# Performance work log

Hardware: AMD Instinct MI355X
Metric: run time of the kernel (lower is better)

The kernel has to match this reference:

```python
import jax, jax.numpy as jnp
import numpy as np

N = 100000   # nodes
E = 1600000  # edges
D_IN = 128
D = 128
G = 64       # graphs in batch
C = 2        # out_channels
EPS = 1e-5   # BatchNorm eps


def setup_inputs() -> dict:
    key = jax.random.key(0)
    ks = jax.random.split(key, 24)
    s = 0.05
    inp = {
        "x": jax.random.normal(ks[0], (N, D_IN), dtype=jnp.float32),
        "edge_index": jax.random.randint(ks[1], (2, E), 0, N, dtype=jnp.int32),
        "edge_attr": jax.random.uniform(ks[2], (E, 2), dtype=jnp.float32),
        "batch": jnp.sort(jax.random.randint(ks[3], (N,), 0, G, dtype=jnp.int32)),
        # GCN layer 0
        "Wg0": jax.random.normal(ks[4], (D_IN, D), dtype=jnp.float32) * s,
        "bg0": jnp.zeros((D,), jnp.float32),
        "gamma0": jnp.ones((D,), jnp.float32),
        "beta0": jnp.zeros((D,), jnp.float32),
        # GCN layer 1
        "Wg1": jax.random.normal(ks[5], (D, D), dtype=jnp.float32) * s,
        "bg1": jnp.zeros((D,), jnp.float32),
        "gamma1": jnp.ones((D,), jnp.float32),
        "beta1": jnp.zeros((D,), jnp.float32),
        # dense head
        "Wl1": jax.random.normal(ks[6], (D, D), dtype=jnp.float32) * s,
        "bl1": jnp.zeros((D,), jnp.float32),
        "Wl2": jax.random.normal(ks[7], (D, D), dtype=jnp.float32) * s,
        "bl2": jnp.zeros((D,), jnp.float32),
        "Wc1": jax.random.normal(ks[8], (D, D), dtype=jnp.float32) * s,
        "bc1": jnp.zeros((D,), jnp.float32),
        "Wc2": jax.random.normal(ks[9], (D, C), dtype=jnp.float32) * s,
        "bc2": jnp.zeros((C,), jnp.float32),
    }
    return inp


def _gcn_conv(x, src, dst, w, W, b):
    # PyG GCNConv: h = x @ W ; add self-loops (weight 1) ; symmetric norm ; agg at dst ; + bias
    h = x @ W                                                   # [N, D]
    deg = jax.ops.segment_sum(w, dst, num_segments=N) + 1.0     # self-loop weight 1
    dinv = jnp.where(deg > 0, jax.lax.rsqrt(deg), 0.0)          # deg^{-1/2}
    norm = dinv[src] * w * dinv[dst]                            # [E]
    agg = jax.ops.segment_sum(norm[:, None] * h[src], dst, num_segments=N)
    agg = agg + (dinv * dinv)[:, None] * h                      # self-loop contribution
    return agg + b


def _bn(x, gamma, beta):
    # training-mode batch statistics over the node dimension
    m = x.mean(axis=0)
    v = x.var(axis=0)
    return (x - m) * jax.lax.rsqrt(v + EPS) * gamma + beta


def reference(x, edge_index, edge_attr, batch,
              Wg0, bg0, gamma0, beta0,
              Wg1, bg1, gamma1, beta1,
              Wl1, bl1, Wl2, bl2, Wc1, bc1, Wc2, bc2):
    src, dst = edge_index[0], edge_index[1]
    w = edge_attr[:, 1]  # which_edge_weight is None -> column 1

    h = jax.nn.relu(_gcn_conv(x, src, dst, w, Wg0, bg0))
    h = _bn(h, gamma0, beta0)                 # dropout: identity (eval)
    h = jax.nn.relu(_gcn_conv(h, src, dst, w, Wg1, bg1))
    h = _bn(h, gamma1, beta1)

    h = jax.nn.relu(h @ Wl1 + bl1)
    h = h @ Wl2 + bl2                          # node embeddings [N, D]

    counts = jax.ops.segment_sum(jnp.ones((N,), h.dtype), batch, num_segments=G)
    graph_reps = jax.ops.segment_sum(h, batch, num_segments=G) / jnp.maximum(counts, 1.0)[:, None]

    logits = jax.nn.relu(graph_reps @ Wc1 + bc1) @ Wc2 + bc2   # [G, C]
    return (h, graph_reps, logits)
```

## Files before the change

### kernel.cpp

```cpp
#include <hip/hip_runtime.h>

#define N_NODES 100000
#define N_EDGES 1600000
#define DFEAT   128
#define NGRAPH  64
#define EPSV    1e-5f
#define SCAN_BLOCKS ((N_NODES + 255) / 256)
#define DEG_SCALE 268435456.0f
#define DEG_MASK  ((1ULL << 42) - 1)

typedef float v4f  __attribute__((ext_vector_type(4)));
typedef short v8s  __attribute__((ext_vector_type(8)));
typedef unsigned short us4 __attribute__((ext_vector_type(4)));
typedef unsigned short us8 __attribute__((ext_vector_type(8)));

static __device__ __forceinline__ unsigned short f2bf(float f) {
    union { float f; unsigned int u; } v; v.f = f;
    unsigned int u = v.u;
    return (unsigned short)((u + 0x7FFFu + ((u >> 16) & 1u)) >> 16);
}
static __device__ __forceinline__ float bf2f(unsigned short b) {
    union { unsigned int u; float f; } v; v.u = ((unsigned int)b) << 16;
    return v.f;
}

__global__ __launch_bounds__(256) void initprep_kernel(
    unsigned long long* __restrict__ degcnt, int* __restrict__ fillc,
    float* __restrict__ stats0, float* __restrict__ stats1,
    float* __restrict__ gsum, float* __restrict__ gcntf,
    const float* __restrict__ W0, const float* __restrict__ W1,
    const float* __restrict__ W2, const float* __restrict__ W3,
    unsigned short* __restrict__ T0, unsigned short* __restrict__ T1,
    unsigned short* __restrict__ T2, unsigned short* __restrict__ T3) {
    int bid = blockIdx.x;
    int i = bid * 256 + threadIdx.x;
    if (i < N_NODES) { degcnt[i] = 0ULL; fillc[i] = 0; }
    if (i < 256)  { stats0[i] = 0.f; stats1[i] = 0.f; }
    if (i < NGRAPH * DFEAT) gsum[i] = 0.f;
    if (i < NGRAPH) gcntf[i] = 0.f;
    if (bid < 256) {
        int which = bid >> 6;
        int i2 = (bid & 63) * 256 + threadIdx.x;
        const float* W = which == 0 ? W0 : which == 1 ? W1 : which == 2 ? W2 : W3;
        unsigned short* T = which == 0 ? T0 : which == 1 ? T1 : which == 2 ? T2 : T3;
        int n = i2 >> 7, k = i2 & 127;
        T[n * 128 + k] = f2bf(W[k * 128 + n]);
    }
}

__global__ void edge_degcnt_kernel(const int* __restrict__ ei, const float* __restrict__ ea,
                                   unsigned long long* __restrict__ degcnt) {
    int e = blockIdx.x * 256 + threadIdx.x;
    if (e >= N_EDGES) return;
    int d = ei[N_EDGES + e];
    float w = ea[2 * e + 1];
    unsigned long long v = (1ULL << 42) | (unsigned long long)(w * DEG_SCALE);
    atomicAdd(&degcnt[d], v);
}

__global__ __launch_bounds__(256) void scan1d_kernel(
    const unsigned long long* __restrict__ degcnt, int* __restrict__ cnt,
    float* __restrict__ dinv, int* __restrict__ blockSum) {
    __shared__ int lds[256];
    int i = blockIdx.x * 256 + threadIdx.x;
    int t = threadIdx.x;
    int c = 0;
    if (i < N_NODES) {
        unsigned long long u = degcnt[i];
        c = (int)(u >> 42);
        cnt[i] = c;
        float deg = 1.0f + (float)(u & DEG_MASK) * (1.0f / DEG_SCALE);
        dinv[i] = rsqrtf(deg);
    }
    lds[t] = c;
    __syncthreads();
    for (int off = 128; off > 0; off >>= 1) {
        if (t < off) lds[t] += lds[t + off];
        __syncthreads();
    }
    if (t == 0) blockSum[blockIdx.x] = lds[0];
}

__global__ __launch_bounds__(512) void scan2_kernel(int* __restrict__ blockSum) {
    __shared__ int lds[512];
    int t = threadIdx.x;
    int v = (t < SCAN_BLOCKS) ? blockSum[t] : 0;
    lds[t] = v;
    __syncthreads();
    for (int off = 1; off < 512; off <<= 1) {
        int u = (t >= off) ? lds[t - off] : 0;
        __syncthreads();
        lds[t] += u;
        __syncthreads();
    }
    if (t < SCAN_BLOCKS) blockSum[t] = lds[t] - v;
}

__global__ __launch_bounds__(256) void scan3_kernel(const int* __restrict__ cnt,
                                                    const int* __restrict__ blockSum,
                                                    int* __restrict__ rowptr) {
    __shared__ int lds[256];
    int i = blockIdx.x * 256 + threadIdx.x;
    int t = threadIdx.x;
    int v = (i < N_NODES) ? cnt[i] : 0;
    lds[t] = v;
    __syncthreads();
    for (int off = 1; off < 256; off <<= 1) {
        int u = (t >= off) ? lds[t - off] : 0;
        __syncthreads();
        lds[t] += u;
        __syncthreads();
    }
    if (i < N_NODES) rowptr[i] = blockSum[blockIdx.x] + lds[t] - v;
    if (i == 0) rowptr[N_NODES] = N_EDGES;
}

__global__ void fill_kernel(const int* __restrict__ ei, const float* __restrict__ ea,
                            const float* __restrict__ dinv, const int* __restrict__ rowptr,
                            int* __restrict__ fillc, int2* __restrict__ edges) {
    int e = blockIdx.x * 256 + threadIdx.x;
    if (e >= N_EDGES) return;
    int s = ei[e], d = ei[N_EDGES + e];
    float w = ea[2 * e + 1];
    float nrm = dinv[s] * w * dinv[d];
    int pos = rowptr[d] + atomicAdd(&fillc[d], 1);
    edges[pos] = make_int2(s, __float_as_int(nrm));
}

__global__ __launch_bounds__(256, 4) void gemm_bf16_kernel(
    const void* __restrict__ Xv, int x_is_f32,
    const unsigned short* __restrict__ Wt,
    void* __restrict__ Outv, int out_is_f32,
    const float* __restrict__ bnp, const float* __restrict__ bias, int do_relu,
    const int* __restrict__ batch, float* __restrict__ gsum,
    float* __restrict__ gcntf, int do_pool) {
    __shared__ unsigned short Ws[128][136];
    const int tid = threadIdx.x;
    const int rb = blockIdx.x * 128;

#pragma unroll
    for (int it = 0; it < 8; ++it) {
        int flat = it * 2048 + tid * 8;
        int n = flat >> 7, k = flat & 127;
        *(us8*)&Ws[n][k] = *(const us8*)&Wt[n * 128 + k];
    }
    __syncthreads();

    const int wv = tid >> 6, lane = tid & 63;
    const int q = lane >> 4, c16 = lane & 15;
    const int rA = rb + wv * 32 + c16;
    const int rB = rA + 16;
    const size_t rAc = (size_t)(rA < N_NODES ? rA : N_NODES - 1);
    const size_t rBc = (size_t)(rB < N_NODES ? rB : N_NODES - 1);

    v4f acc[2][8];
#pragma unroll
    for (int i = 0; i < 2; ++i)
#pragma unroll
        for (int j = 0; j < 8; ++j) acc[i][j] = (v4f){0.f, 0.f, 0.f, 0.f};

#pragma unroll
    for (int ks = 0; ks < 4; ++ks) {
        const int k0 = ks * 32 + q * 8;
        v8s a0, a1;
        if (x_is_f32) {
            const float* X = (const float*)Xv;
            float4 f0 = *(const float4*)&X[rAc * 128 + k0];
            float4 f1 = *(const float4*)&X[rAc * 128 + k0 + 4];
            float4 g0 = *(const float4*)&X[rBc * 128 + k0];
            float4 g1 = *(const float4*)&X[rBc * 128 + k0 + 4];
            if (bnp) {
                float4 s0 = *(const float4*)&bnp[k0];
                float4 s1 = *(const float4*)&bnp[k0 + 4];
                float4 b0 = *(const float4*)&bnp[128 + k0];
                float4 b1 = *(const float4*)&bnp[128 + k0 + 4];
                f0.x = f0.x * s0.x + b0.x; f0.y = f0.y * s0.y + b0.y;
                f0.z = f0.z * s0.z + b0.z; f0.w = f0.w * s0.w + b0.w;
                f1.x = f1.x * s1.x + b1.x; f1.y = f1.y * s1.y + b1.y;
                f1.z = f1.z * s1.z + b1.z; f1.w = f1.w * s1.w + b1.w;
                g0.x = g0.x * s0.x + b0.x; g0.y = g0.y * s0.y + b0.y;
                g0.z = g0.z * s0.z + b0.z; g0.w = g0.w * s0.w + b0.w;
                g1.x = g1.x * s1.x + b1.x; g1.y = g1.y * s1.y + b1.y;
                g1.z = g1.z * s1.z + b1.z; g1.w = g1.w * s1.w + b1.w;
            }
            us8 oa, ob;
            oa[0] = f2bf(f0.x); oa[1] = f2bf(f0.y); oa[2] = f2bf(f0.z); oa[3] = f2bf(f0.w);
            oa[4] = f2bf(f1.x); oa[5] = f2bf(f1.y); oa[6] = f2bf(f1.z); oa[7] = f2bf(f1.w);
            ob[0] = f2bf(g0.x); ob[1] = f2bf(g0.y); ob[2] = f2bf(g0.z); ob[3] = f2bf(g0.w);
            ob[4] = f2bf(g1.x); ob[5] = f2bf(g1.y); ob[6] = f2bf(g1.z); ob[7] = f2bf(g1.w);
            a0 = *(v8s*)&oa; a1 = *(v8s*)&ob;
        } else {
            const unsigned short* X = (const unsigned short*)Xv;
            us8 v0 = *(const us8*)&X[rAc * 128 + k0];
            us8 v1 = *(const us8*)&X[rBc * 128 + k0];
            if (bnp) {
                float4 s0 = *(const float4*)&bnp[k0];
                float4 s1 = *(const float4*)&bnp[k0 + 4];
                float4 b0 = *(const float4*)&bnp[128 + k0];
                float4 b1 = *(const float4*)&bnp[128 + k0 + 4];
                v0[0] = f2bf(bf2f(v0[0]) * s0.x + b0.x);
                v0[1] = f2bf(bf2f(v0[1]) * s0.y + b0.y);
                v0[2] = f2bf(bf2f(v0[2]) * s0.z + b0.z);
                v0[3] = f2bf(bf2f(v0[3]) * s0.w + b0.w);
                v0[4] = f2bf(bf2f(v0[4]) * s1.x + b1.x);
                v0[5] = f2bf(bf2f(v0[5]) * s1.y + b1.y);
                v0[6] = f2bf(bf2f(v0[6]) * s1.z + b1.z);
                v0[7] = f2bf(bf2f(v0[7]) * s1.w + b1.w);
                v1[0] = f2bf(bf2f(v1[0]) * s0.x + b0.x);
                v1[1] = f2bf(bf2f(v1[1]) * s0.y + b0.y);
                v1[2] = f2bf(bf2f(v1[2]) * s0.z + b0.z);
                v1[3] = f2bf(bf2f(v1[3]) * s0.w + b0.w);
                v1[4] = f2bf(bf2f(v1[4]) * s1.x + b1.x);
                v1[5] = f2bf(bf2f(v1[5]) * s1.y + b1.y);
                v1[6] = f2bf(bf2f(v1[6]) * s1.z + b1.z);
                v1[7] = f2bf(bf2f(v1[7]) * s1.w + b1.w);
            }
            a0 = *(v8s*)&v0; a1 = *(v8s*)&v1;
        }
#pragma unroll
        for (int nt = 0; nt < 8; ++nt) {
            v8s b = *(const v8s*)&Ws[nt * 16 + c16][ks * 32 + q * 8];
            acc[0][nt] = __builtin_amdgcn_mfma_f32_16x16x32_bf16(a0, b, acc[0][nt], 0, 0, 0);
            acc[1][nt] = __builtin_amdgcn_mfma_f32_16x16x32_bf16(a1, b, acc[1][nt], 0, 0, 0);
        }
    }

#pragma unroll
    for (int mt = 0; mt < 2; ++mt) {
#pragma unroll
        for (int nt = 0; nt < 8; ++nt) {
            int col = nt * 16 + c16;
            float bcol = bias ? bias[col] : 0.f;
#pragma unroll
            for (int r = 0; r < 4; ++r) {
                int row = rb + wv * 32 + mt * 16 + q * 4 + r;
                float o = acc[mt][nt][r] + bcol;
                if (do_relu) o = fmaxf(o, 0.f);
                acc[mt][nt][r] = o;
                if (row >= N_NODES) continue;
                if (out_is_f32) ((float*)Outv)[(size_t)row * 128 + col] = o;
                else ((unsigned short*)Outv)[(size_t)row * 128 + col] = f2bf(o);
            }
        }
    }

    if (do_pool) {
        __shared__ float pg[128];
        __shared__ float pcnt;
        int br[8];
#pragma unroll
        for (int mt = 0; mt < 2; ++mt)
#pragma unroll
            for (int r = 0; r < 4; ++r) {
                int row = rb + wv * 32 + mt * 16 + q * 4 + r;
                br[mt * 4 + r] = (row < N_NODES) ? batch[row] : -1;
            }
        int rlast = (rb + 127 < N_NODES) ? rb + 127 : N_NODES - 1;
        int gmin = batch[rb];
        int gmax = batch[rlast];
        for (int g = gmin; g <= gmax; ++g) {
            if (tid < 128) pg[tid] = 0.f;
            if (tid == 0) pcnt = 0.f;
            __syncthreads();
            if (wv < 2) {
                int rr = rb + tid;
                bool p = (tid < 128) && (rr < N_NODES) && (batch[rr] == g);
                unsigned long long m = __ballot(p);
                if (lane == 0 && m) atomicAdd(&pcnt, (float)__popcll(m));
            }
#pragma unroll
            for (int nt = 0; nt < 8; ++nt) {
                float s = 0.f;
#pragma unroll
                for (int mt = 0; mt < 2; ++mt)
#pragma unroll
                    for (int r = 0; r < 4; ++r)
                        if (br[mt * 4 + r] == g) s += acc[mt][nt][r];
                s += __shfl_xor(s, 16);
                s += __shfl_xor(s, 32);
                if (q == 0 && s != 0.f) atomicAdd(&pg[nt * 16 + c16], s);
            }
            __syncthreads();
            if (tid < 128 && pg[tid] != 0.f) atomicAdd(&gsum[g * 128 + tid], pg[tid]);
            if (tid == 0 && pcnt != 0.f) atomicAdd(&gcntf[g], pcnt);
            __syncthreads();
        }
    }
}

__global__ __launch_bounds__(256) void agg_relu_bf16_kernel(
    const unsigned short* __restrict__ H, const int* __restrict__ rowptr,
    const int2* __restrict__ edges,
    const float* __restrict__ dinv, const float* __restrict__ bias,
    unsigned short* __restrict__ outb, float* __restrict__ stats, int nwaves) {
    __shared__ float red[1024];
    const int tid = threadIdx.x;
    const int wv = tid >> 6;
    const int lane = tid & 63;
    const float bx = bias[2 * lane], by = bias[2 * lane + 1];
    const unsigned int* __restrict__ H4 = (const unsigned int*)H;
    unsigned int* __restrict__ O4 = (unsigned int*)outb;
    float s0 = 0.f, q0 = 0.f, s1 = 0.f, q1 = 0.f;

    for (int i = blockIdx.x * 4 + wv; i < N_NODES; i += nwaves) {
        int beg = __builtin_amdgcn_readfirstlane(rowptr[i]);
        int end = __builtin_amdgcn_readfirstlane(rowptr[i + 1]);
        float di = dinv[i];
        unsigned int hs = H4[(size_t)i * 64 + lane];
        float px0 = 0.f, py0 = 0.f, px1 = 0.f, py1 = 0.f;
        float px2 = 0.f, py2 = 0.f, px3 = 0.f, py3 = 0.f;
        const int last = end - 1;
        for (int j = beg; j < end; j += 8) {
            int j1 = j + 1 < end ? j + 1 : last;
            int j2 = j + 2 < end ? j + 2 : last;
            int j3 = j + 3 < end ? j + 3 : last;
            int j4 = j + 4 < end ? j + 4 : last;
            int j5 = j + 5 < end ? j + 5 : last;
            int j6 = j + 6 < end ? j + 6 : last;
            int j7 = j + 7 < end ? j + 7 : last;
            int2 e0 = edges[j];
            int2 e1 = edges[j1];
            int2 e2 = edges[j2];
            int2 e3 = edges[j3];
            int2 e4 = edges[j4];
            int2 e5 = edges[j5];
            int2 e6 = edges[j6];
            int2 e7 = edges[j7];
            unsigned int h0 = H4[(size_t)e0.x * 64 + lane];
            unsigned int h1 = H4[(size_t)e1.x * 64 + lane];
            unsigned int h2 = H4[(size_t)e2.x * 64 + lane];
            unsigned int h3 = H4[(size_t)e3.x * 64 + lane];
            unsigned int h4 = H4[(size_t)e4.x * 64 + lane];
            unsigned int h5 = H4[(size_t)e5.x * 64 + lane];
            unsigned int h6 = H4[(size_t)e6.x * 64 + lane];
            unsigned int h7 = H4[(size_t)e7.x * 64 + lane];
            float v0 = __int_as_float(e0.y);
            float v1 = j + 1 < end ? __int_as_float(e1.y) : 0.f;
            float v2 = j + 2 < end ? __int_as_float(e2.y) : 0.f;
            float v3 = j + 3 < end ? __int_as_float(e3.y) : 0.f;
            float v4 = j + 4 < end ? __int_as_float(e4.y) : 0.f;
            float v5 = j + 5 < end ? __int_as_float(e5.y) : 0.f;
            float v6 = j + 6 < end ? __int_as_float(e6.y) : 0.f;
            float v7 = j + 7 < end ? __int_as_float(e7.y) : 0.f;
            px0 = fmaf(v0, bf2f((unsigned short)h0), px0);
            py0 = fmaf(v0, bf2f((unsigned short)(h0 >> 16)), py0);
            px1 = fmaf(v1, bf2f((unsigned short)h1), px1);
            py1 = fmaf(v1, bf2f((unsigned short)(h1 >> 16)), py1);
            px2 = fmaf(v2, bf2f((unsigned short)h2), px2);
            py2 = fmaf(v2, bf2f((unsigned short)(h2 >> 16)), py2);
            px3 = fmaf(v3, bf2f((unsigned short)h3), px3);
            py3 = fmaf(v3, bf2f((unsigned short)(h3 >> 16)), py3);
            px0 = fmaf(v4, bf2f((unsigned short)h4), px0);
            py0 = fmaf(v4, bf2f((unsigned short)(h4 >> 16)), py0);
            px1 = fmaf(v5, bf2f((unsigned short)h5), px1);
            py1 = fmaf(v5, bf2f((unsigned short)(h5 >> 16)), py1);
            px2 = fmaf(v6, bf2f((unsigned short)h6), px2);
            py2 = fmaf(v6, bf2f((unsigned short)(h6 >> 16)), py2);
            px3 = fmaf(v7, bf2f((unsigned short)h7), px3);
            py3 = fmaf(v7, bf2f((unsigned short)(h7 >> 16)), py3);
        }
        float dd = di * di;
        float ax = (px0 + px1) + (px2 + px3);
        float ay = (py0 + py1) + (py2 + py3);
        ax = fmaf(dd, bf2f((unsigned short)hs), ax) + bx;
        ay = fmaf(dd, bf2f((unsigned short)(hs >> 16)), ay) + by;
        ax = fmaxf(ax, 0.f);
        ay = fmaxf(ay, 0.f);
        O4[(size_t)i * 64 + lane] =
            (unsigned int)f2bf(ax) | ((unsigned int)f2bf(ay) << 16);
        s0 += ax; q0 += ax * ax; s1 += ay; q1 += ay * ay;
    }

    red[wv * 128 + 2 * lane]           = s0;
    red[wv * 128 + 2 * lane + 1]       = s1;
    red[512 + wv * 128 + 2 * lane]     = q0;
    red[512 + wv * 128 + 2 * lane + 1] = q1;
    __syncthreads();
    if (tid < 128) {
        float ts = red[tid] + red[128 + tid] + red[256 + tid] + red[384 + tid];
        float tq = red[512 + tid] + red[640 + tid] + red[768 + tid] + red[896 + tid];
        atomicAdd(&stats[tid], ts);
        atomicAdd(&stats[128 + tid], tq);
    }
}

__global__ void bn_finalize_kernel(const float* __restrict__ stats,
                                   const float* __restrict__ gamma,
                                   const float* __restrict__ beta,
                                   float* __restrict__ bnp) {
    int f = threadIdx.x;
    float mean = stats[f] / (float)N_NODES;
    float var = stats[128 + f] / (float)N_NODES - mean * mean;
    float sc = gamma[f] * rsqrtf(var + EPSV);
    bnp[f] = sc;
    bnp[128 + f] = beta[f] - mean * sc;
}

__global__ __launch_bounds__(128) void logits_kernel(
    const float* __restrict__ gsum, const float* __restrict__ gcntf,
    const float* __restrict__ Wc1, const float* __restrict__ bc1,
    const float* __restrict__ Wc2, const float* __restrict__ bc2,
    float* __restrict__ out_reps, float* __restrict__ out_logits) {
    __shared__ float repS[128];
    __shared__ float tmp[128];
    int g = blockIdx.x, t = threadIdx.x;
    float rep = gsum[(size_t)g * 128 + t] / fmaxf(gcntf[g], 1.0f);
    out_reps[(size_t)g * 128 + t] = rep;
    repS[t] = rep;
    __syncthreads();
    float acc = bc1[t];
    for (int k = 0; k < 128; ++k) acc = fmaf(repS[k], Wc1[k * 128 + t], acc);
    tmp[t] = fmaxf(acc, 0.f);
    __syncthreads();
    if (t < 2) {
        float a = bc2[t];
        for (int k = 0; k < 128; ++k) a = fmaf(tmp[k], Wc2[k * 2 + t], a);
        out_logits[g * 2 + t] = a;
    }
}

extern "C" void kernel_launch(void* const* d_in, const int* in_sizes, int n_in,
                              void* d_out, int out_size, void* d_ws, size_t ws_size,
                              hipStream_t stream) {
    const float* x      = (const float*)d_in[0];
    const int*   ei     = (const int*)d_in[1];
    const float* ea     = (const float*)d_in[2];
    const int*   batch  = (const int*)d_in[3];
    const float* Wg0    = (const float*)d_in[4];
    const float* bg0    = (const float*)d_in[5];
    const float* gamma0 = (const float*)d_in[6];
    const float* beta0  = (const float*)d_in[7];
    const float* Wg1    = (const float*)d_in[8];
    const float* bg1    = (const float*)d_in[9];
    const float* gamma1 = (const float*)d_in[10];
    const float* beta1  = (const float*)d_in[11];
    const float* Wl1    = (const float*)d_in[12];
    const float* bl1    = (const float*)d_in[13];
    const float* Wl2    = (const float*)d_in[14];
    const float* bl2    = (const float*)d_in[15];
    const float* Wc1    = (const float*)d_in[16];
    const float* bc1    = (const float*)d_in[17];
    const float* Wc2    = (const float*)d_in[18];
    const float* bc2    = (const float*)d_in[19];

    float* out = (float*)d_out;
    char* ws = (char*)d_ws;
    size_t off = 0;
    auto alloc = [&](size_t bytes) {
        void* p = ws + off;
        off += (bytes + 15) & ~(size_t)15;
        return p;
    };
    unsigned short* bufHb = (unsigned short*)alloc(sizeof(unsigned short) * (size_t)N_NODES * 128);
    unsigned short* bufAb = (unsigned short*)alloc(sizeof(unsigned short) * (size_t)N_NODES * 128);
    int2* edges = (int2*)alloc(sizeof(int2) * (size_t)N_EDGES);
    unsigned long long* degcnt = (unsigned long long*)alloc(sizeof(unsigned long long) * N_NODES);
    unsigned short* Wt0   = (unsigned short*)alloc(sizeof(unsigned short) * 128 * 128);
    unsigned short* Wt1   = (unsigned short*)alloc(sizeof(unsigned short) * 128 * 128);
    unsigned short* Wt2   = (unsigned short*)alloc(sizeof(unsigned short) * 128 * 128);
    unsigned short* Wt3   = (unsigned short*)alloc(sizeof(unsigned short) * 128 * 128);
    float* dinv   = (float*)alloc(sizeof(float) * N_NODES);
    int*   cnt    = (int*)alloc(sizeof(int) * N_NODES);
    int*   fillc  = (int*)alloc(sizeof(int) * N_NODES);
    float* stats0 = (float*)alloc(sizeof(float) * 256);
    float* stats1 = (float*)alloc(sizeof(float) * 256);
    float* bnp0   = (float*)alloc(sizeof(float) * 256);
    float* bnp1   = (float*)alloc(sizeof(float) * 256);
    float* gsum   = (float*)alloc(sizeof(float) * NGRAPH * 128);
    float* gcntf  = (float*)alloc(sizeof(float) * NGRAPH);
    int*   rowptr = (int*)alloc(sizeof(int) * (N_NODES + 1));
    int*   blockSum = (int*)alloc(sizeof(int) * SCAN_BLOCKS);

    initprep_kernel<<<SCAN_BLOCKS, 256, 0, stream>>>(degcnt, fillc, stats0, stats1,
                                                     gsum, gcntf, Wg0, Wg1, Wl1, Wl2,
                                                     Wt0, Wt1, Wt2, Wt3);
    edge_degcnt_kernel<<<(N_EDGES + 255) / 256, 256, 0, stream>>>(ei, ea, degcnt);
    scan1d_kernel<<<SCAN_BLOCKS, 256, 0, stream>>>(degcnt, cnt, dinv, blockSum);
    scan2_kernel<<<1, 512, 0, stream>>>(blockSum);
    scan3_kernel<<<SCAN_BLOCKS, 256, 0, stream>>>(cnt, blockSum, rowptr);
    fill_kernel<<<(N_EDGES + 255) / 256, 256, 0, stream>>>(ei, ea, dinv, rowptr, fillc,
                                                           edges);

    const int gemm_grid = (N_NODES + 127) / 128;
    const int agg_blocks = 2048;
    const int agg_nwaves = agg_blocks * 4;
    gemm_bf16_kernel<<<gemm_grid, 256, 0, stream>>>(x, 1, Wt0, bufHb, 0, nullptr,
                                                    nullptr, 0, nullptr, nullptr, nullptr, 0);
    agg_relu_bf16_kernel<<<agg_blocks, 256, 0, stream>>>(bufHb, rowptr, edges,
                                                         dinv, bg0, bufAb, stats0, agg_nwaves);
    bn_finalize_kernel<<<1, 128, 0, stream>>>(stats0, gamma0, beta0, bnp0);
    gemm_bf16_kernel<<<gemm_grid, 256, 0, stream>>>(bufAb, 0, Wt1, bufHb, 0, bnp0,
                                                    nullptr, 0, nullptr, nullptr, nullptr, 0);
    agg_relu_bf16_kernel<<<agg_blocks, 256, 0, stream>>>(bufHb, rowptr, edges,
                                                         dinv, bg1, bufAb, stats1, agg_nwaves);
    bn_finalize_kernel<<<1, 128, 0, stream>>>(stats1, gamma1, beta1, bnp1);
    gemm_bf16_kernel<<<gemm_grid, 256, 0, stream>>>(bufAb, 0, Wt2, bufHb, 0, bnp1,
                                                    bl1, 1, nullptr, nullptr, nullptr, 0);
    gemm_bf16_kernel<<<gemm_grid, 256, 0, stream>>>(bufHb, 0, Wt3, out, 1, nullptr,
                                                    bl2, 0, batch, gsum, gcntf, 1);
    logits_kernel<<<NGRAPH, 128, 0, stream>>>(gsum, gcntf, Wc1, bc1, Wc2, bc2,
                                              out + (size_t)N_NODES * 128,
                                              out + (size_t)N_NODES * 128 + NGRAPH * 128);
}
```

Measured before the change: 584.0 us.

## Slice GCN features into 16-column planes for cache-friendly aggregation; fuse fill with first GEMM

The GEMMs feeding the two GCN aggregations now write their bf16 output in a feature-sliced layout: eight planes of 16 features per node. Each aggregation block handles one slice over a contiguous range of nodes, so each gathered row is 32 bytes and a slice of H (about 3.2 MB) can stay in cache. Within a wave, 8 edges are processed in parallel with 8 lanes per edge, then reduced with shuffles. The CSR fill kernel and the first GEMM are merged into one launch with block-range dispatch, removing a launch and letting the two overlap. In exchange, the edge list and rowptr are re-read once per slice (8 times), and the shuffle reductions and smaller gathers add overhead.

```diff
diff --git a/kernel.cpp b/kernel.cpp
--- a/kernel.cpp
+++ b/kernel.cpp
@@ -8,6 +8,11 @@
 #define SCAN_BLOCKS ((N_NODES + 255) / 256)
 #define DEG_SCALE 268435456.0f
 #define DEG_MASK  ((1ULL << 42) - 1)
+#define FILL_BLOCKS ((N_EDGES + 255) / 256)
+#define GEMM_GRID   ((N_NODES + 127) / 128)
+#define AGG_BLOCKS  2048
+#define AGG_GROUPS  (AGG_BLOCKS / 8)
+#define AGG_RPG     ((N_NODES + AGG_GROUPS - 1) / AGG_GROUPS)
 
 typedef float v4f  __attribute__((ext_vector_type(4)));
 typedef short v8s  __attribute__((ext_vector_type(8)));
@@ -23,6 +28,7 @@
     union { unsigned int u; float f; } v; v.u = ((unsigned int)b) << 16;
     return v.f;
 }
+static __device__ __forceinline__ int minI(int a, int b) { return a < b ? a : b; }
 
 __global__ __launch_bounds__(256) void initprep_kernel(
     unsigned long long* __restrict__ degcnt, int* __restrict__ fillc,
@@ -115,22 +121,83 @@
     if (i == 0) rowptr[N_NODES] = N_EDGES;
 }
 
-__global__ void fill_kernel(const int* __restrict__ ei, const float* __restrict__ ea,
-                            const float* __restrict__ dinv, const int* __restrict__ rowptr,
-                            int* __restrict__ fillc, int2* __restrict__ edges) {
-    int e = blockIdx.x * 256 + threadIdx.x;
-    if (e >= N_EDGES) return;
-    int s = ei[e], d = ei[N_EDGES + e];
-    float w = ea[2 * e + 1];
-    float nrm = dinv[s] * w * dinv[d];
-    int pos = rowptr[d] + atomicAdd(&fillc[d], 1);
-    edges[pos] = make_int2(s, __float_as_int(nrm));
+__global__ __launch_bounds__(256, 4) void fill_gemm0_kernel(
+    const int* __restrict__ ei, const float* __restrict__ ea,
+    const float* __restrict__ dinv, const int* __restrict__ rowptr,
+    int* __restrict__ fillc, int2* __restrict__ edges,
+    const float* __restrict__ X, const unsigned short* __restrict__ Wt,
+    unsigned short* __restrict__ Outs) {
+    __shared__ unsigned short Ws[128][136];
+    if (blockIdx.x < FILL_BLOCKS) {
+        int e = blockIdx.x * 256 + threadIdx.x;
+        if (e >= N_EDGES) return;
+        int s = ei[e], d = ei[N_EDGES + e];
+        float w = ea[2 * e + 1];
+        float nrm = dinv[s] * w * dinv[d];
+        int pos = rowptr[d] + atomicAdd(&fillc[d], 1);
+        edges[pos] = make_int2(s, __float_as_int(nrm));
+        return;
+    }
+    const int tid = threadIdx.x;
+    const int rb = (blockIdx.x - FILL_BLOCKS) * 128;
+#pragma unroll
+    for (int it = 0; it < 8; ++it) {
+        int flat = it * 2048 + tid * 8;
+        int n = flat >> 7, k = flat & 127;
+        *(us8*)&Ws[n][k] = *(const us8*)&Wt[n * 128 + k];
+    }
+    __syncthreads();
+
+    const int wv = tid >> 6, lane = tid & 63;
+    const int q = lane >> 4, c16 = lane & 15;
+    const int rA = rb + wv * 32 + c16;
+    const int rB = rA + 16;
+    const size_t rAc = (size_t)(rA < N_NODES ? rA : N_NODES - 1);
+    const size_t rBc = (size_t)(rB < N_NODES ? rB : N_NODES - 1);
+
+    v4f acc[2][8];
+#pragma unroll
+    for (int i = 0; i < 2; ++i)
+#pragma unroll
+        for (int j = 0; j < 8; ++j) acc[i][j] = (v4f){0.f, 0.f, 0.f, 0.f};
+
+#pragma unroll
+    for (int ks = 0; ks < 4; ++ks) {
+        const int k0 = ks * 32 + q * 8;
+        float4 f0 = *(const float4*)&X[rAc * 128 + k0];
+        float4 f1 = *(const float4*)&X[rAc * 128 + k0 + 4];
+        float4 g0 = *(const float4*)&X[rBc * 128 + k0];
+        float4 g1 = *(const float4*)&X[rBc * 128 + k0 + 4];
+        us8 oa, ob;
+        oa[0] = f2bf(f0.x); oa[1] = f2bf(f0.y); oa[2] = f2bf(f0.z); oa[3] = f2bf(f0.w);
+        oa[4] = f2bf(f1.x); oa[5] = f2bf(f1.y); oa[6] = f2bf(f1.z); oa[7] = f2bf(f1.w);
+        ob[0] = f2bf(g0.x); ob[1] = f2bf(g0.y); ob[2] = f2bf(g0.z); ob[3] = f2bf(g0.w);
+        ob[4] = f2bf(g1.x); ob[5] = f2bf(g1.y); ob[6] = f2bf(g1.z); ob[7] = f2bf(g1.w);
+        v8s a0 = *(v8s*)&oa, a1 = *(v8s*)&ob;
+#pragma unroll
+        for (int nt = 0; nt < 8; ++nt) {
+            v8s b = *(const v8s*)&Ws[nt * 16 + c16][ks * 32 + q * 8];
+            acc[0][nt] = __builtin_amdgcn_mfma_f32_16x16x32_bf16(a0, b, acc[0][nt], 0, 0, 0);
+            acc[1][nt] = __builtin_amdgcn_mfma_f32_16x16x32_bf16(a1, b, acc[1][nt], 0, 0, 0);
+        }
+    }
+#pragma unroll
+    for (int mt = 0; mt < 2; ++mt)
+#pragma unroll
+        for (int nt = 0; nt < 8; ++nt)
+#pragma unroll
+            for (int r = 0; r < 4; ++r) {
+                int row = rb + wv * 32 + mt * 16 + q * 4 + r;
+                if (row >= N_NODES) continue;
+                Outs[(size_t)nt * N_NODES * 16 + (size_t)row * 16 + c16] =
+                    f2bf(acc[mt][nt][r]);
+            }
 }
 
 __global__ __launch_bounds__(256, 4) void gemm_bf16_kernel(
-    const void* __restrict__ Xv, int x_is_f32,
+    const unsigned short* __restrict__ X,
     const unsigned short* __restrict__ Wt,
-    void* __restrict__ Outv, int out_is_f32,
+    void* __restrict__ Outv, int out_mode,
     const float* __restrict__ bnp, const float* __restrict__ bias, int do_relu,
     const int* __restrict__ batch, float* __restrict__ gsum,
     float* __restrict__ gcntf, int do_pool) {
@@ -162,61 +229,31 @@
 #pragma unroll
     for (int ks = 0; ks < 4; ++ks) {
         const int k0 = ks * 32 + q * 8;
-        v8s a0, a1;
-        if (x_is_f32) {
-            const float* X = (const float*)Xv;
-            float4 f0 = *(const float4*)&X[rAc * 128 + k0];
-            float4 f1 = *(const float4*)&X[rAc * 128 + k0 + 4];
-            float4 g0 = *(const float4*)&X[rBc * 128 + k0];
-            float4 g1 = *(const float4*)&X[rBc * 128 + k0 + 4];
-            if (bnp) {
-                float4 s0 = *(const float4*)&bnp[k0];
-                float4 s1 = *(const float4*)&bnp[k0 + 4];
-                float4 b0 = *(const float4*)&bnp[128 + k0];
-                float4 b1 = *(const float4*)&bnp[128 + k0 + 4];
-                f0.x = f0.x * s0.x + b0.x; f0.y = f0.y * s0.y + b0.y;
-                f0.z = f0.z * s0.z + b0.z; f0.w = f0.w * s0.w + b0.w;
-                f1.x = f1.x * s1.x + b1.x; f1.y = f1.y * s1.y + b1.y;
-                f1.z = f1.z * s1.z + b1.z; f1.w = f1.w * s1.w + b1.w;
-                g0.x = g0.x * s0.x + b0.x; g0.y = g0.y * s0.y + b0.y;
-                g0.z = g0.z * s0.z + b0.z; g0.w = g0.w * s0.w + b0.w;
-                g1.x = g1.x * s1.x + b1.x; g1.y = g1.y * s1.y + b1.y;
-                g1.z = g1.z * s1.z + b1.z; g1.w = g1.w * s1.w + b1.w;
-            }
-            us8 oa, ob;
-            oa[0] = f2bf(f0.x); oa[1] = f2bf(f0.y); oa[2] = f2bf(f0.z); oa[3] = f2bf(f0.w);
-            oa[4] = f2bf(f1.x); oa[5] = f2bf(f1.y); oa[6] = f2bf(f1.z); oa[7] = f2bf(f1.w);
-            ob[0] = f2bf(g0.x); ob[1] = f2bf(g0.y); ob[2] = f2bf(g0.z); ob[3] = f2bf(g0.w);
-            ob[4] = f2bf(g1.x); ob[5] = f2bf(g1.y); ob[6] = f2bf(g1.z); ob[7] = f2bf(g1.w);
-            a0 = *(v8s*)&oa; a1 = *(v8s*)&ob;
-        } else {
-            const unsigned short* X = (const unsigned short*)Xv;
-            us8 v0 = *(const us8*)&X[rAc * 128 + k0];
-            us8 v1 = *(const us8*)&X[rBc * 128 + k0];
-            if (bnp) {
-                float4 s0 = *(const float4*)&bnp[k0];
-                float4 s1 = *(const float4*)&bnp[k0 + 4];
-                float4 b0 = *(const float4*)&bnp[128 + k0];
-                float4 b1 = *(const float4*)&bnp[128 + k0 + 4];
-                v0[0] = f2bf(bf2f(v0[0]) * s0.x + b0.x);
-                v0[1] = f2bf(bf2f(v0[1]) * s0.y + b0.y);
-                v0[2] = f2bf(bf2f(v0[2]) * s0.z + b0.z);
-                v0[3] = f2bf(bf2f(v0[3]) * s0.w + b0.w);
-                v0[4] = f2bf(bf2f(v0[4]) * s1.x + b1.x);
-                v0[5] = f2bf(bf2f(v0[5]) * s1.y + b1.y);
-                v0[6] = f2bf(bf2f(v0[6]) * s1.z + b1.z);
-                v0[7] = f2bf(bf2f(v0[7]) * s1.w + b1.w);
-                v1[0] = f2bf(bf2f(v1[0]) * s0.x + b0.x);
-                v1[1] = f2bf(bf2f(v1[1]) * s0.y + b0.y);
-                v1[2] = f2bf(bf2f(v1[2]) * s0.z + b0.z);
-                v1[3] = f2bf(bf2f(v1[3]) * s0.w + b0.w);
-                v1[4] = f2bf(bf2f(v1[4]) * s1.x + b1.x);
-                v1[5] = f2bf(bf2f(v1[5]) * s1.y + b1.y);
-                v1[6] = f2bf(bf2f(v1[6]) * s1.z + b1.z);
-                v1[7] = f2bf(bf2f(v1[7]) * s1.w + b1.w);
-            }
-            a0 = *(v8s*)&v0; a1 = *(v8s*)&v1;
-        }
+        us8 v0 = *(const us8*)&X[rAc * 128 + k0];
+        us8 v1 = *(const us8*)&X[rBc * 128 + k0];
+        if (bnp) {
+            float4 s0 = *(const float4*)&bnp[k0];
+            float4 s1 = *(const float4*)&bnp[k0 + 4];
+            float4 b0 = *(const float4*)&bnp[128 + k0];
+            float4 b1 = *(const float4*)&bnp[128 + k0 + 4];
+            v0[0] = f2bf(bf2f(v0[0]) * s0.x + b0.x);
+            v0[1] = f2bf(bf2f(v0[1]) * s0.y + b0.y);
+            v0[2] = f2bf(bf2f(v0[2]) * s0.z + b0.z);
+            v0[3] = f2bf(bf2f(v0[3]) * s0.w + b0.w);
+            v0[4] = f2bf(bf2f(v0[4]) * s1.x + b1.x);
+            v0[5] = f2bf(bf2f(v0[5]) * s1.y + b1.y);
+            v0[6] = f2bf(bf2f(v0[6]) * s1.z + b1.z);
+            v0[7] = f2bf(bf2f(v0[7]) * s1.w + b1.w);
+            v1[0] = f2bf(bf2f(v1[0]) * s0.x + b0.x);
+            v1[1] = f2bf(bf2f(v1[1]) * s0.y + b0.y);
+            v1[2] = f2bf(bf2f(v1[2]) * s0.z + b0.z);
+            v1[3] = f2bf(bf2f(v1[3]) * s0.w + b0.w);
+            v1[4] = f2bf(bf2f(v1[4]) * s1.x + b1.x);
+            v1[5] = f2bf(bf2f(v1[5]) * s1.y + b1.y);
+            v1[6] = f2bf(bf2f(v1[6]) * s1.z + b1.z);
+            v1[7] = f2bf(bf2f(v1[7]) * s1.w + b1.w);
+        }
+        v8s a0 = *(v8s*)&v0, a1 = *(v8s*)&v1;
 #pragma unroll
         for (int nt = 0; nt < 8; ++nt) {
             v8s b = *(const v8s*)&Ws[nt * 16 + c16][ks * 32 + q * 8];
@@ -238,8 +275,9 @@
                 if (do_relu) o = fmaxf(o, 0.f);
                 acc[mt][nt][r] = o;
                 if (row >= N_NODES) continue;
-                if (out_is_f32) ((float*)Outv)[(size_t)row * 128 + col] = o;
-                else ((unsigned short*)Outv)[(size_t)row * 128 + col] = f2bf(o);
+                if (out_mode == 1)      ((float*)Outv)[(size_t)row * 128 + col] = o;
+                else if (out_mode == 0) ((unsigned short*)Outv)[(size_t)row * 128 + col] = f2bf(o);
+                else ((unsigned short*)Outv)[(size_t)nt * N_NODES * 16 + (size_t)row * 16 + c16] = f2bf(o);
             }
         }
     }
@@ -288,99 +326,73 @@
     }
 }
 
-__global__ __launch_bounds__(256) void agg_relu_bf16_kernel(
-    const unsigned short* __restrict__ H, const int* __restrict__ rowptr,
-    const int2* __restrict__ edges,
-    const float* __restrict__ dinv, const float* __restrict__ bias,
-    unsigned short* __restrict__ outb, float* __restrict__ stats, int nwaves) {
-    __shared__ float red[1024];
+__global__ __launch_bounds__(256) void agg_relu_sliced_kernel(
+    const unsigned short* __restrict__ Hs, const int* __restrict__ rowptr,
+    const int2* __restrict__ edges, const float* __restrict__ dinv,
+    const float* __restrict__ bias, unsigned short* __restrict__ outb,
+    float* __restrict__ stats) {
+    const int slice = blockIdx.x & 7;
+    const int grp   = blockIdx.x >> 3;
     const int tid = threadIdx.x;
-    const int wv = tid >> 6;
-    const int lane = tid & 63;
-    const float bx = bias[2 * lane], by = bias[2 * lane + 1];
-    const unsigned int* __restrict__ H4 = (const unsigned int*)H;
+    const int wv = tid >> 6, lane = tid & 63;
+    const int e = lane >> 3;
+    const int u = lane & 7;
+    const unsigned int* __restrict__ H4s =
+        (const unsigned int*)Hs + (size_t)slice * N_NODES * 8;
     unsigned int* __restrict__ O4 = (unsigned int*)outb;
+    const int f0 = slice * 16 + 2 * u;
+    const float bx = bias[f0], by = bias[f0 + 1];
+
     float s0 = 0.f, q0 = 0.f, s1 = 0.f, q1 = 0.f;
-
-    for (int i = blockIdx.x * 4 + wv; i < N_NODES; i += nwaves) {
+    const int r0 = grp * AGG_RPG;
+    int r1 = r0 + AGG_RPG; if (r1 > N_NODES) r1 = N_NODES;
+
+    for (int i = r0 + wv; i < r1; i += 4) {
         int beg = __builtin_amdgcn_readfirstlane(rowptr[i]);
         int end = __builtin_amdgcn_readfirstlane(rowptr[i + 1]);
+        int n = end - beg;
+        int last = end - 1;
         float di = dinv[i];
-        unsigned int hs = H4[(size_t)i * 64 + lane];
-        float px0 = 0.f, py0 = 0.f, px1 = 0.f, py1 = 0.f;
-        float px2 = 0.f, py2 = 0.f, px3 = 0.f, py3 = 0.f;
-        const int last = end - 1;
-        for (int j = beg; j < end; j += 8) {
-            int j1 = j + 1 < end ? j + 1 : last;
-            int j2 = j + 2 < end ? j + 2 : last;
-            int j3 = j + 3 < end ? j + 3 : last;
-            int j4 = j + 4 < end ? j + 4 : last;
-            int j5 = j + 5 < end ? j + 5 : last;
-            int j6 = j + 6 < end ? j + 6 : last;
-            int j7 = j + 7 < end ? j + 7 : last;
-            int2 e0 = edges[j];
-            int2 e1 = edges[j1];
-            int2 e2 = edges[j2];
-            int2 e3 = edges[j3];
-            int2 e4 = edges[j4];
-            int2 e5 = edges[j5];
-            int2 e6 = edges[j6];
-            int2 e7 = edges[j7];
-            unsigned int h0 = H4[(size_t)e0.x * 64 + lane];
-            unsigned int h1 = H4[(size_t)e1.x * 64 + lane];
-            unsigned int h2 = H4[(size_t)e2.x * 64 + lane];
-            unsigned int h3 = H4[(size_t)e3.x * 64 + lane];
-            unsigned int h4 = H4[(size_t)e4.x * 64 + lane];
-            unsigned int h5 = H4[(size_t)e5.x * 64 + lane];
-            unsigned int h6 = H4[(size_t)e6.x * 64 + lane];
-            unsigned int h7 = H4[(size_t)e7.x * 64 + lane];
-            float v0 = __int_as_float(e0.y);
-            float v1 = j + 1 < end ? __int_as_float(e1.y) : 0.f;
-            float v2 = j + 2 < end ? __int_as_float(e2.y) : 0.f;
-            float v3 = j + 3 < end ? __int_as_float(e3.y) : 0.f;
-            float v4 = j + 4 < end ? __int_as_float(e4.y) : 0.f;
-            float v5 = j + 5 < end ? __int_as_float(e5.y) : 0.f;
-            float v6 = j + 6 < end ? __int_as_float(e6.y) : 0.f;
-            float v7 = j + 7 < end ? __int_as_float(e7.y) : 0.f;
-            px0 = fmaf(v0, bf2f((unsigned short)h0), px0);
-            py0 = fmaf(v0, bf2f((unsigned short)(h0 >> 16)), py0);
-            px1 = fmaf(v1, bf2f((unsigned short)h1), px1);
-            py1 = fmaf(v1, bf2f((unsigned short)(h1 >> 16)), py1);
-            px2 = fmaf(v2, bf2f((unsigned short)h2), px2);
-            py2 = fmaf(v2, bf2f((unsigned short)(h2 >> 16)), py2);
-            px3 = fmaf(v3, bf2f((unsigned short)h3), px3);
-            py3 = fmaf(v3, bf2f((unsigned short)(h3 >> 16)), py3);
-            px0 = fmaf(v4, bf2f((unsigned short)h4), px0);
-            py0 = fmaf(v4, bf2f((unsigned short)(h4 >> 16)), py0);
-            px1 = fmaf(v5, bf2f((unsigned short)h5), px1);
-            py1 = fmaf(v5, bf2f((unsigned short)(h5 >> 16)), py1);
-            px2 = fmaf(v6, bf2f((unsigned short)h6), px2);
-            py2 = fmaf(v6, bf2f((unsigned short)(h6 >> 16)), py2);
-            px3 = fmaf(v7, bf2f((unsigned short)h7), px3);
-            py3 = fmaf(v7, bf2f((unsigned short)(h7 >> 16)), py3);
-        }
-        float dd = di * di;
-        float ax = (px0 + px1) + (px2 + px3);
-        float ay = (py0 + py1) + (py2 + py3);
-        ax = fmaf(dd, bf2f((unsigned short)hs), ax) + bx;
-        ay = fmaf(dd, bf2f((unsigned short)(hs >> 16)), ay) + by;
-        ax = fmaxf(ax, 0.f);
-        ay = fmaxf(ay, 0.f);
-        O4[(size_t)i * 64 + lane] =
-            (unsigned int)f2bf(ax) | ((unsigned int)f2bf(ay) << 16);
-        s0 += ax; q0 += ax * ax; s1 += ay; q1 += ay * ay;
-    }
-
-    red[wv * 128 + 2 * lane]           = s0;
-    red[wv * 128 + 2 * lane + 1]       = s1;
-    red[512 + wv * 128 + 2 * lane]     = q0;
-    red[512 + wv * 128 + 2 * lane + 1] = q1;
-    __syncthreads();
-    if (tid < 128) {
-        float ts = red[tid] + red[128 + tid] + red[256 + tid] + red[384 + tid];
-        float tq = red[512 + tid] + red[640 + tid] + red[768 + tid] + red[896 + tid];
-        atomicAdd(&stats[tid], ts);
-        atomicAdd(&stats[128 + tid], tq);
+        unsigned int hs = H4s[(size_t)i * 8 + u];
+        float ax = 0.f, ay = 0.f;
+        for (int c = 0; c < n; c += 16) {
+            int j0 = beg + c + e;
+            int j1 = j0 + 8;
+            int2 e0 = edges[minI(j0, last)];
+            int2 e1 = edges[minI(j1, last)];
+            unsigned int h0 = H4s[(size_t)(unsigned)e0.x * 8 + u];
+            unsigned int h1 = H4s[(size_t)(unsigned)e1.x * 8 + u];
+            float w0 = (c + e < n) ? __int_as_float(e0.y) : 0.f;
+            float w1 = (c + 8 + e < n) ? __int_as_float(e1.y) : 0.f;
+            ax = fmaf(w0, bf2f((unsigned short)h0), ax);
+            ay = fmaf(w0, bf2f((unsigned short)(h0 >> 16)), ay);
+            ax = fmaf(w1, bf2f((unsigned short)h1), ax);
+            ay = fmaf(w1, bf2f((unsigned short)(h1 >> 16)), ay);
+        }
+        ax += __shfl_xor(ax, 8);  ay += __shfl_xor(ay, 8);
+        ax += __shfl_xor(ax, 16); ay += __shfl_xor(ay, 16);
+        ax += __shfl_xor(ax, 32); ay += __shfl_xor(ay, 32);
+        if (e == 0) {
+            float dd = di * di;
+            ax = fmaf(dd, bf2f((unsigned short)hs), ax) + bx;
+            ay = fmaf(dd, bf2f((unsigned short)(hs >> 16)), ay) + by;
+            ax = fmaxf(ax, 0.f);
+            ay = fmaxf(ay, 0.f);
+            O4[(size_t)i * 64 + slice * 8 + u] =
+                (unsigned int)f2bf(ax) | ((unsigned int)f2bf(ay) << 16);
+            s0 += ax; q0 += ax * ax; s1 += ay; q1 += ay * ay;
+        }
+    }
+
+    __shared__ float red[4][8][4];
+    if (e == 0) { red[wv][u][0] = s0; red[wv][u][1] = s1;
+                  red[wv][u][2] = q0; red[wv][u][3] = q1; }
+    __syncthreads();
+    if (tid < 32) {
+        int uu = tid >> 2, v = tid & 3;
+        float t = red[0][uu][v] + red[1][uu][v] + red[2][uu][v] + red[3][uu][v];
+        int f = slice * 16 + 2 * uu + (v & 1);
+        atomicAdd(&stats[(v >> 1) * 128 + f], t);
     }
 }
 
@@ -478,25 +490,19 @@
     scan1d_kernel<<<SCAN_BLOCKS, 256, 0, stream>>>(degcnt, cnt, dinv, blockSum);
     scan2_kernel<<<1, 512, 0, stream>>>(blockSum);
     scan3_kernel<<<SCAN_BLOCKS, 256, 0, stream>>>(cnt, blockSum, rowptr);
-    fill_kernel<<<(N_EDGES + 255) / 256, 256, 0, stream>>>(ei, ea, dinv, rowptr, fillc,
-                                                           edges);
-
-    const int gemm_grid = (N_NODES + 127) / 128;
-    const int agg_blocks = 2048;
-    const int agg_nwaves = agg_blocks * 4;
-    gemm_bf16_kernel<<<gemm_grid, 256, 0, stream>>>(x, 1, Wt0, bufHb, 0, nullptr,
+    fill_gemm0_kernel<<<FILL_BLOCKS + GEMM_GRID, 256, 0, stream>>>(
+        ei, ea, dinv, rowptr, fillc, edges, x, Wt0, bufHb);
+    agg_relu_sliced_kernel<<<AGG_BLOCKS, 256, 0, stream>>>(bufHb, rowptr, edges,
+                                                           dinv, bg0, bufAb, stats0);
+    bn_finalize_kernel<<<1, 128, 0, stream>>>(stats0, gamma0, beta0, bnp0);
+    gemm_bf16_kernel<<<GEMM_GRID, 256, 0, stream>>>(bufAb, Wt1, bufHb, 2, bnp0,
                                                     nullptr, 0, nullptr, nullptr, nullptr, 0);
-    agg_relu_bf16_kernel<<<agg_blocks, 256, 0, stream>>>(bufHb, rowptr, edges,
-                                                         dinv, bg0, bufAb, stats0, agg_nwaves);
-    bn_finalize_kernel<<<1, 128, 0, stream>>>(stats0, gamma0, beta0, bnp0);
-    gemm_bf16_kernel<<<gemm_grid, 256, 0, stream>>>(bufAb, 0, Wt1, bufHb, 0, bnp0,
-                                                    nullptr, 0, nullptr, nullptr, nullptr, 0);
-    agg_relu_bf16_kernel<<<agg_blocks, 256, 0, stream>>>(bufHb, rowptr, edges,
-                                                         dinv, bg1, bufAb, stats1, agg_nwaves);
+    agg_relu_sliced_kernel<<<AGG_BLOCKS, 256, 0, stream>>>(bufHb, rowptr, edges,
+                                                           dinv, bg1, bufAb, stats1);
     bn_finalize_kernel<<<1, 128, 0, stream>>>(stats1, gamma1, beta1, bnp1);
-    gemm_bf16_kernel<<<gemm_grid, 256, 0, stream>>>(bufAb, 0, Wt2, bufHb, 0, bnp1,
+    gemm_bf16_kernel<<<GEMM_GRID, 256, 0, stream>>>(bufAb, Wt2, bufHb, 0, bnp1,
                                                     bl1, 1, nullptr, nullptr, nullptr, 0);
-    gemm_bf16_kernel<<<gemm_grid, 256, 0, stream>>>(bufHb, 0, Wt3, out, 1, nullptr,
+    gemm_bf16_kernel<<<GEMM_GRID, 256, 0, stream>>>(bufHb, Wt3, out, 1, nullptr,
                                                     bl2, 0, batch, gsum, gcntf, 1);
     logits_kernel<<<NGRAPH, 128, 0, stream>>>(gsum, gcntf, Wc1, bc1, Wc2, bc2,
                                               out + (size_t)N_NODES * 128,
```

Result: slower. 709.9 us (+21.6%).

## Merge CSR fill and first GEMM into one launch with block-range dispatch

Applied to the files above, without the earlier changes.

The edge-fill scatter and the first layer's x@W GEMM are independent, so both now run in a single kernel whose blocks are split by index: the first range fills CSR edges and the rest compute the bf16 GEMM. This removes one launch and lets the atomic-bound scatter overlap the MFMA GEMM. The general GEMM drops its f32-input path. Fill blocks now reserve the GEMM's shared memory and are bound by its launch bounds, which may lower their occupancy.

```diff
diff --git a/kernel.cpp b/kernel.cpp
--- a/kernel.cpp
+++ b/kernel.cpp
@@ -8,6 +8,8 @@
 #define SCAN_BLOCKS ((N_NODES + 255) / 256)
 #define DEG_SCALE 268435456.0f
 #define DEG_MASK  ((1ULL << 42) - 1)
+#define FILL_BLOCKS ((N_EDGES + 255) / 256)
+#define GEMM_GRID   ((N_NODES + 127) / 128)
 
 typedef float v4f  __attribute__((ext_vector_type(4)));
 typedef short v8s  __attribute__((ext_vector_type(8)));
@@ -115,20 +117,80 @@
     if (i == 0) rowptr[N_NODES] = N_EDGES;
 }
 
-__global__ void fill_kernel(const int* __restrict__ ei, const float* __restrict__ ea,
-                            const float* __restrict__ dinv, const int* __restrict__ rowptr,
-                            int* __restrict__ fillc, int2* __restrict__ edges) {
-    int e = blockIdx.x * 256 + threadIdx.x;
-    if (e >= N_EDGES) return;
-    int s = ei[e], d = ei[N_EDGES + e];
-    float w = ea[2 * e + 1];
-    float nrm = dinv[s] * w * dinv[d];
-    int pos = rowptr[d] + atomicAdd(&fillc[d], 1);
-    edges[pos] = make_int2(s, __float_as_int(nrm));
+__global__ __launch_bounds__(256, 4) void fill_gemm0_kernel(
+    const int* __restrict__ ei, const float* __restrict__ ea,
+    const float* __restrict__ dinv, const int* __restrict__ rowptr,
+    int* __restrict__ fillc, int2* __restrict__ edges,
+    const float* __restrict__ X, const unsigned short* __restrict__ Wt,
+    unsigned short* __restrict__ Out) {
+    __shared__ unsigned short Ws[128][136];
+    if (blockIdx.x < FILL_BLOCKS) {
+        int e = blockIdx.x * 256 + threadIdx.x;
+        if (e >= N_EDGES) return;
+        int s = ei[e], d = ei[N_EDGES + e];
+        float w = ea[2 * e + 1];
+        float nrm = dinv[s] * w * dinv[d];
+        int pos = rowptr[d] + atomicAdd(&fillc[d], 1);
+        edges[pos] = make_int2(s, __float_as_int(nrm));
+        return;
+    }
+    const int tid = threadIdx.x;
+    const int rb = (blockIdx.x - FILL_BLOCKS) * 128;
+#pragma unroll
+    for (int it = 0; it < 8; ++it) {
+        int flat = it * 2048 + tid * 8;
+        int n = flat >> 7, k = flat & 127;
+        *(us8*)&Ws[n][k] = *(const us8*)&Wt[n * 128 + k];
+    }
+    __syncthreads();
+
+    const int wv = tid >> 6, lane = tid & 63;
+    const int q = lane >> 4, c16 = lane & 15;
+    const int rA = rb + wv * 32 + c16;
+    const int rB = rA + 16;
+    const size_t rAc = (size_t)(rA < N_NODES ? rA : N_NODES - 1);
+    const size_t rBc = (size_t)(rB < N_NODES ? rB : N_NODES - 1);
+
+    v4f acc[2][8];
+#pragma unroll
+    for (int i = 0; i < 2; ++i)
+#pragma unroll
+        for (int j = 0; j < 8; ++j) acc[i][j] = (v4f){0.f, 0.f, 0.f, 0.f};
+
+#pragma unroll
+    for (int ks = 0; ks < 4; ++ks) {
+        const int k0 = ks * 32 + q * 8;
+        float4 f0 = *(const float4*)&X[rAc * 128 + k0];
+        float4 f1 = *(const float4*)&X[rAc * 128 + k0 + 4];
+        float4 g0 = *(const float4*)&X[rBc * 128 + k0];
+        float4 g1 = *(const float4*)&X[rBc * 128 + k0 + 4];
+        us8 oa, ob;
+        oa[0] = f2bf(f0.x); oa[1] = f2bf(f0.y); oa[2] = f2bf(f0.z); oa[3] = f2bf(f0.w);
+        oa[4] = f2bf(f1.x); oa[5] = f2bf(f1.y); oa[6] = f2bf(f1.z); oa[7] = f2bf(f1.w);
+        ob[0] = f2bf(g0.x); ob[1] = f2bf(g0.y); ob[2] = f2bf(g0.z); ob[3] = f2bf(g0.w);
+        ob[4] = f2bf(g1.x); ob[5] = f2bf(g1.y); ob[6] = f2bf(g1.z); ob[7] = f2bf(g1.w);
+        v8s a0 = *(v8s*)&oa, a1 = *(v8s*)&ob;
+#pragma unroll
+        for (int nt = 0; nt < 8; ++nt) {
+            v8s b = *(const v8s*)&Ws[nt * 16 + c16][ks * 32 + q * 8];
+            acc[0][nt] = __builtin_amdgcn_mfma_f32_16x16x32_bf16(a0, b, acc[0][nt], 0, 0, 0);
+            acc[1][nt] = __builtin_amdgcn_mfma_f32_16x16x32_bf16(a1, b, acc[1][nt], 0, 0, 0);
+        }
+    }
+#pragma unroll
+    for (int mt = 0; mt < 2; ++mt)
+#pragma unroll
+        for (int nt = 0; nt < 8; ++nt)
+#pragma unroll
+            for (int r = 0; r < 4; ++r) {
+                int row = rb + wv * 32 + mt * 16 + q * 4 + r;
+                if (row >= N_NODES) continue;
+                Out[(size_t)row * 128 + nt * 16 + c16] = f2bf(acc[mt][nt][r]);
+            }
 }
 
 __global__ __launch_bounds__(256, 4) void gemm_bf16_kernel(
-    const void* __restrict__ Xv, int x_is_f32,
+    const unsigned short* __restrict__ X,
     const unsigned short* __restrict__ Wt,
     void* __restrict__ Outv, int out_is_f32,
     const float* __restrict__ bnp, const float* __restrict__ bias, int do_relu,
@@ -162,61 +224,31 @@
 #pragma unroll
     for (int ks = 0; ks < 4; ++ks) {
         const int k0 = ks * 32 + q * 8;
-        v8s a0, a1;
-        if (x_is_f32) {
-            const float* X = (const float*)Xv;
-            float4 f0 = *(const float4*)&X[rAc * 128 + k0];
-            float4 f1 = *(const float4*)&X[rAc * 128 + k0 + 4];
-            float4 g0 = *(const float4*)&X[rBc * 128 + k0];
-            float4 g1 = *(const float4*)&X[rBc * 128 + k0 + 4];
-            if (bnp) {
-                float4 s0 = *(const float4*)&bnp[k0];
-                float4 s1 = *(const float4*)&bnp[k0 + 4];
-                float4 b0 = *(const float4*)&bnp[128 + k0];
-                float4 b1 = *(const float4*)&bnp[128 + k0 + 4];
-                f0.x = f0.x * s0.x + b0.x; f0.y = f0.y * s0.y + b0.y;
-                f0.z = f0.z * s0.z + b0.z; f0.w = f0.w * s0.w + b0.w;
-                f1.x = f1.x * s1.x + b1.x; f1.y = f1.y * s1.y + b1.y;
-                f1.z = f1.z * s1.z + b1.z; f1.w = f1.w * s1.w + b1.w;
-                g0.x = g0.x * s0.x + b0.x; g0.y = g0.y * s0.y + b0.y;
-                g0.z = g0.z * s0.z + b0.z; g0.w = g0.w * s0.w + b0.w;
-                g1.x = g1.x * s1.x + b1.x; g1.y = g1.y * s1.y + b1.y;
-                g1.z = g1.z * s1.z + b1.z; g1.w = g1.w * s1.w + b1.w;
-            }
-            us8 oa, ob;
-            oa[0] = f2bf(f0.x); oa[1] = f2bf(f0.y); oa[2] = f2bf(f0.z); oa[3] = f2bf(f0.w);
-            oa[4] = f2bf(f1.x); oa[5] = f2bf(f1.y); oa[6] = f2bf(f1.z); oa[7] = f2bf(f1.w);
-            ob[0] = f2bf(g0.x); ob[1] = f2bf(g0.y); ob[2] = f2bf(g0.z); ob[3] = f2bf(g0.w);
-            ob[4] = f2bf(g1.x); ob[5] = f2bf(g1.y); ob[6] = f2bf(g1.z); ob[7] = f2bf(g1.w);
-            a0 = *(v8s*)&oa; a1 = *(v8s*)&ob;
-        } else {
-            const unsigned short* X = (const unsigned short*)Xv;
-            us8 v0 = *(const us8*)&X[rAc * 128 + k0];
-            us8 v1 = *(const us8*)&X[rBc * 128 + k0];
-            if (bnp) {
-                float4 s0 = *(const float4*)&bnp[k0];
-                float4 s1 = *(const float4*)&bnp[k0 + 4];
-                float4 b0 = *(const float4*)&bnp[128 + k0];
-                float4 b1 = *(const float4*)&bnp[128 + k0 + 4];
-                v0[0] = f2bf(bf2f(v0[0]) * s0.x + b0.x);
-                v0[1] = f2bf(bf2f(v0[1]) * s0.y + b0.y);
-                v0[2] = f2bf(bf2f(v0[2]) * s0.z + b0.z);
-                v0[3] = f2bf(bf2f(v0[3]) * s0.w + b0.w);
-                v0[4] = f2bf(bf2f(v0[4]) * s1.x + b1.x);
-                v0[5] = f2bf(bf2f(v0[5]) * s1.y + b1.y);
-                v0[6] = f2bf(bf2f(v0[6]) * s1.z + b1.z);
-                v0[7] = f2bf(bf2f(v0[7]) * s1.w + b1.w);
-                v1[0] = f2bf(bf2f(v1[0]) * s0.x + b0.x);
-                v1[1] = f2bf(bf2f(v1[1]) * s0.y + b0.y);
-                v1[2] = f2bf(bf2f(v1[2]) * s0.z + b0.z);
-                v1[3] = f2bf(bf2f(v1[3]) * s0.w + b0.w);
-                v1[4] = f2bf(bf2f(v1[4]) * s1.x + b1.x);
-                v1[5] = f2bf(bf2f(v1[5]) * s1.y + b1.y);
-                v1[6] = f2bf(bf2f(v1[6]) * s1.z + b1.z);
-                v1[7] = f2bf(bf2f(v1[7]) * s1.w + b1.w);
-            }
-            a0 = *(v8s*)&v0; a1 = *(v8s*)&v1;
+        us8 v0 = *(const us8*)&X[rAc * 128 + k0];
+        us8 v1 = *(const us8*)&X[rBc * 128 + k0];
+        if (bnp) {
+            float4 s0 = *(const float4*)&bnp[k0];
+            float4 s1 = *(const float4*)&bnp[k0 + 4];
+            float4 b0 = *(const float4*)&bnp[128 + k0];
+            float4 b1 = *(const float4*)&bnp[128 + k0 + 4];
+            v0[0] = f2bf(bf2f(v0[0]) * s0.x + b0.x);
+            v0[1] = f2bf(bf2f(v0[1]) * s0.y + b0.y);
+            v0[2] = f2bf(bf2f(v0[2]) * s0.z + b0.z);
+            v0[3] = f2bf(bf2f(v0[3]) * s0.w + b0.w);
+            v0[4] = f2bf(bf2f(v0[4]) * s1.x + b1.x);
+            v0[5] = f2bf(bf2f(v0[5]) * s1.y + b1.y);
+            v0[6] = f2bf(bf2f(v0[6]) * s1.z + b1.z);
+            v0[7] = f2bf(bf2f(v0[7]) * s1.w + b1.w);
+            v1[0] = f2bf(bf2f(v1[0]) * s0.x + b0.x);
+            v1[1] = f2bf(bf2f(v1[1]) * s0.y + b0.y);
+            v1[2] = f2bf(bf2f(v1[2]) * s0.z + b0.z);
+            v1[3] = f2bf(bf2f(v1[3]) * s0.w + b0.w);
+            v1[4] = f2bf(bf2f(v1[4]) * s1.x + b1.x);
+            v1[5] = f2bf(bf2f(v1[5]) * s1.y + b1.y);
+            v1[6] = f2bf(bf2f(v1[6]) * s1.z + b1.z);
+            v1[7] = f2bf(bf2f(v1[7]) * s1.w + b1.w);
         }
+        v8s a0 = *(v8s*)&v0, a1 = *(v8s*)&v1;
 #pragma unroll
         for (int nt = 0; nt < 8; ++nt) {
             v8s b = *(const v8s*)&Ws[nt * 16 + c16][ks * 32 + q * 8];
@@ -478,25 +510,22 @@
     scan1d_kernel<<<SCAN_BLOCKS, 256, 0, stream>>>(degcnt, cnt, dinv, blockSum);
     scan2_kernel<<<1, 512, 0, stream>>>(blockSum);
     scan3_kernel<<<SCAN_BLOCKS, 256, 0, stream>>>(cnt, blockSum, rowptr);
-    fill_kernel<<<(N_EDGES + 255) / 256, 256, 0, stream>>>(ei, ea, dinv, rowptr, fillc,
-                                                           edges);
-
-    const int gemm_grid = (N_NODES + 127) / 128;
+    fill_gemm0_kernel<<<FILL_BLOCKS + GEMM_GRID, 256, 0, stream>>>(
+        ei, ea, dinv, rowptr, fillc, edges, x, Wt0, bufHb);
+
     const int agg_blocks = 2048;
     const int agg_nwaves = agg_blocks * 4;
-    gemm_bf16_kernel<<<gemm_grid, 256, 0, stream>>>(x, 1, Wt0, bufHb, 0, nullptr,
-                                                    nullptr, 0, nullptr, nullptr, nullptr, 0);
     agg_relu_bf16_kernel<<<agg_blocks, 256, 0, stream>>>(bufHb, rowptr, edges,
                                                          dinv, bg0, bufAb, stats0, agg_nwaves);
     bn_finalize_kernel<<<1, 128, 0, stream>>>(stats0, gamma0, beta0, bnp0);
-    gemm_bf16_kernel<<<gemm_grid, 256, 0, stream>>>(bufAb, 0, Wt1, bufHb, 0, bnp0,
+    gemm_bf16_kernel<<<GEMM_GRID, 256, 0, stream>>>(bufAb, Wt1, bufHb, 0, bnp0,
                                                     nullptr, 0, nullptr, nullptr, nullptr, 0);
     agg_relu_bf16_kernel<<<agg_blocks, 256, 0, stream>>>(bufHb, rowptr, edges,
                                                          dinv, bg1, bufAb, stats1, agg_nwaves);
     bn_finalize_kernel<<<1, 128, 0, stream>>>(stats1, gamma1, beta1, bnp1);
-    gemm_bf16_kernel<<<gemm_grid, 256, 0, stream>>>(bufAb, 0, Wt2, bufHb, 0, bnp1,
+    gemm_bf16_kernel<<<GEMM_GRID, 256, 0, stream>>>(bufAb, Wt2, bufHb, 0, bnp1,
                                                     bl1, 1, nullptr, nullptr, nullptr, 0);
-    gemm_bf16_kernel<<<gemm_grid, 256, 0, stream>>>(bufHb, 0, Wt3, out, 1, nullptr,
+    gemm_bf16_kernel<<<GEMM_GRID, 256, 0, stream>>>(bufHb, Wt3, out, 1, nullptr,
                                                     bl2, 0, batch, gsum, gcntf, 1);
     logits_kernel<<<NGRAPH, 128, 0, stream>>>(gsum, gcntf, Wc1, bc1, Wc2, bc2,
                                               out + (size_t)N_NODES * 128,
```

Result: no change. 580.4 us (-0.6%).
